# Kernel tuning notes

Measured on AMD Instinct MI355X. Metric: run time of the kernel, lower is better.

Reference implementation:

```python
import jax, jax.numpy as jnp
import numpy as np

LAMBDA_SCR = 0.015
LAMBDA_IFD = 0.015


def setup_inputs() -> dict:
    key = jax.random.key(0)
    k = jax.random.split(key, 5)
    pred = jax.random.normal(k[0], (32, 1000), dtype=jnp.float32)
    feat0 = jax.random.normal(k[1], (32, 64, 128, 128), dtype=jnp.float32)
    feat1 = jax.random.normal(k[2], (32, 128, 64, 64), dtype=jnp.float32)
    feat2 = jax.random.normal(k[3], (32, 256, 32, 32), dtype=jnp.float32)  # teacher
    target = jax.random.randint(k[4], (32,), 0, 1000, dtype=jnp.int64)
    return {"pred": pred, "feat0": feat0, "feat1": feat1, "feat2": feat2, "target": target}


def _adaptive_avg_pool2d(x, out_hw):
    # Exact-multiple adaptive average pool (matches torch for integer ratios).
    B, C, H, W = x.shape
    Ho, Wo = out_hw
    if Ho >= H:
        x = jnp.repeat(x, Ho // H, axis=2)  # replication upsample
    else:
        x = x.reshape(B, C, Ho, H // Ho, W).mean(axis=3)
    if Wo >= W:
        x = jnp.repeat(x, Wo // W, axis=3)
    else:
        x = x.reshape(B, C, x.shape[2], Wo, W // Wo).mean(axis=4)
    return x


def _random_channel_selection(feat, target_channels, key):
    C = feat.shape[1]
    if C == target_channels:
        return feat
    idx = jax.random.permutation(key, C)[:target_channels]
    return feat[:, idx, :, :]


def _ifd_loss(feat):
    B, C, H, W = feat.shape
    if C < 2:
        return jnp.float32(0.0)
    # L2 norm per channel -> descending sort of channel indices
    norms = jnp.linalg.norm(feat.reshape(B, C, H * W), axis=-1)  # [B, C]
    idx = jnp.argsort(-norms, axis=1)                            # [B, C]
    half = C // 2
    strong = jnp.take_along_axis(feat, idx[:, :half, None, None], axis=1)
    weak = jnp.take_along_axis(feat, idx[:, half:2 * half, None, None], axis=1)
    A_strong = jax.nn.sigmoid(strong.mean(axis=1))  # [B, H, W]
    A_weak = jax.nn.sigmoid(weak.mean(axis=1))
    # sum_b mean_hw(diff^2) / B == mean over all elements
    return jnp.mean((A_weak - jax.lax.stop_gradient(A_strong)) ** 2)


def reference(pred, feat0, feat1, feat2, target):
    logp = jax.nn.log_softmax(pred, axis=-1)
    l_main = -jnp.mean(jnp.take_along_axis(logp, target[:, None], axis=1))

    features = [feat0, feat1, feat2]
    teacher = features[-1]
    students = features[:-1]

    sel_key = jax.random.key(42)  # fixed keys stand in for torch.randperm
    l_scr = jnp.float32(0.0)
    for i, student in enumerate(students):
        t_down = _adaptive_avg_pool2d(teacher, student.shape[2:])
        min_C = min(teacher.shape[1], student.shape[1])
        ks, kt = jax.random.split(jax.random.fold_in(sel_key, i))
        s_aligned = _random_channel_selection(student, min_C, ks)
        t_aligned = _random_channel_selection(t_down, min_C, kt)
        l_scr = l_scr + jnp.mean((s_aligned - jax.lax.stop_gradient(t_aligned)) ** 2)
    l_scr = l_scr / len(students)

    l_ifd = jnp.float32(0.0)
    for feat in features:
        l_ifd = l_ifd + _ifd_loss(feat)
    l_ifd = l_ifd / len(features)

    total = l_main + LAMBDA_SCR * l_scr + LAMBDA_IFD * l_ifd
    return (total, l_main, l_scr, l_ifd)
```

## Files before the change

### kernel.cpp

```cpp
#include <hip/hip_runtime.h>
#include <stdint.h>
#include <math.h>

__device__ __forceinline__ void tf_block(uint32_t k0, uint32_t k1, uint32_t& x0, uint32_t& x1) {
  uint32_t k2 = 0x1BD11BDAu ^ k0 ^ k1;
  x0 += k0; x1 += k1;
#define TFR(r) { x0 += x1; x1 = (x1 << r) | (x1 >> (32 - r)); x1 ^= x0; }
  TFR(13) TFR(15) TFR(26) TFR(6)
  x0 += k1; x1 += k2 + 1u;
  TFR(17) TFR(29) TFR(16) TFR(24)
  x0 += k2; x1 += k0 + 2u;
  TFR(13) TFR(15) TFR(26) TFR(6)
  x0 += k0; x1 += k1 + 3u;
  TFR(17) TFR(29) TFR(16) TFR(24)
  x0 += k1; x1 += k2 + 4u;
  TFR(13) TFR(15) TFR(26) TFR(6)
  x0 += k2; x1 += k0 + 5u;
#undef TFR
}

__device__ __forceinline__ float sigmoidf(float x) { return 1.0f / (1.0f + expf(-x)); }

__device__ __forceinline__ float block_reduce(float v, float* red) {
  __syncthreads();
  int lane = threadIdx.x & 63, wv = threadIdx.x >> 6;
  for (int o = 32; o > 0; o >>= 1) v += __shfl_down(v, o, 64);
  if (lane == 0) red[wv] = v;
  __syncthreads();
  float r = 0.f;
  if (threadIdx.x == 0) r = red[0] + red[1] + red[2] + red[3];
  return r;
}

__global__ __launch_bounds__(256) void k0_perm(int* idx0, int* idx1, float* ws, float* totz) {
  int t = threadIdx.x;
  if (blockIdx.x > 0) {
    float4 z = {0.f, 0.f, 0.f, 0.f};
    ((float4*)totz)[(blockIdx.x - 1) * 256 + t] = z;
    return;
  }
  __shared__ uint32_t sub[2][2];
  __shared__ uint32_t bits[2][256];
  for (int i = t; i < 384; i += 256) ws[i] = 0.0f;
  if (t == 0) {
    for (int i = 0; i < 2; ++i) {
      uint32_t f0 = 0u, f1 = (uint32_t)i;
      tf_block(0u, 42u, f0, f1);
      uint32_t a0 = 0u, a1 = 2u; tf_block(f0, f1, a0, a1);
      uint32_t b0 = 1u, b1 = 3u; tf_block(f0, f1, b0, b1);
      uint32_t kt0 = a1, kt1 = b1;
      uint32_t c0 = 0u, c1 = 2u; tf_block(kt0, kt1, c0, c1);
      uint32_t d0 = 1u, d1 = 3u; tf_block(kt0, kt1, d0, d1);
      sub[i][0] = c1; sub[i][1] = d1;
    }
  }
  __syncthreads();
  if (t < 128) {
    for (int i = 0; i < 2; ++i) {
      uint32_t x0 = (uint32_t)t, x1 = (uint32_t)(t + 128);
      tf_block(sub[i][0], sub[i][1], x0, x1);
      bits[i][t] = x0; bits[i][t + 128] = x1;
    }
  }
  __syncthreads();
  for (int i = 0; i < 2; ++i) {
    uint32_t mine = bits[i][t];
    int rank = 0;
    for (int k = 0; k < 256; ++k) {
      uint32_t v = bits[i][k];
      rank += (v < mine) || (v == mine && k < t);
    }
    int lim = (i == 0) ? 64 : 128;
    if (rank < lim) { (i == 0 ? idx0 : idx1)[rank] = t; }
  }
}

template<bool WT>
__global__ __launch_bounds__(256) void k1_pass1(
    const float* __restrict__ f0, const float* __restrict__ f1, const float* __restrict__ f2,
    const int* __restrict__ idx0, const int* __restrict__ idx1,
    float* __restrict__ ns0p, float* __restrict__ ns1p, float* __restrict__ ns2p,
    float* __restrict__ scr0_s, float* __restrict__ scr1_s,
    float* __restrict__ tot0, float* __restrict__ tot1, float* __restrict__ tot2) {
  __shared__ float nsp[16 * 256];
  __shared__ int sidx[128];
  __shared__ float red[8];
  int bid = blockIdx.x, t = threadIdx.x;
  int lane = t & 63, wv = t >> 6;

  if (bid < 2048) {
    int q = bid, b = q >> 6, r = q & 63, chunk = r >> 2, cg = r & 3;
    if (t < 64) sidx[t] = idx0[t];
    __syncthreads();
    const float* fb = f0 + (size_t)b * 1048576 + (size_t)cg * 16 * 16384 + chunk * 1024;
    const float* tb = f2 + (size_t)b * 262144 + (chunk * 2 + (t >> 7)) * 32 + (t & 31);
    float4 tot = {0.f, 0.f, 0.f, 0.f};
    float scr = 0.f;
    #pragma unroll
    for (int c = 0; c < 16; ++c) {
      float4 v = ((const float4*)(fb + (size_t)c * 16384))[t];
      float tv = tb[(size_t)sidx[cg * 16 + c] * 1024];
      tot.x += v.x; tot.y += v.y; tot.z += v.z; tot.w += v.w;
      nsp[c * 256 + t] = v.x * v.x + v.y * v.y + v.z * v.z + v.w * v.w;
      float dx = v.x - tv, dy = v.y - tv, dz = v.z - tv, dw = v.w - tv;
      scr += dx * dx + dy * dy + dz * dz + dw * dw;
    }
    __syncthreads();
    #pragma unroll
    for (int j = 0; j < 4; ++j) {
      int c = wv * 4 + j;
      float s = nsp[c * 256 + lane] + nsp[c * 256 + lane + 64] +
                nsp[c * 256 + lane + 128] + nsp[c * 256 + lane + 192];
      #pragma unroll
      for (int o = 32; o > 0; o >>= 1) s += __shfl_down(s, o, 64);
      if (lane == 0) ns0p[(b * 16 + chunk) * 64 + cg * 16 + c] = s;
    }
    if (WT) {
      float* tp = tot0 + (size_t)b * 16384 + chunk * 1024 + t * 4;
      atomicAdd(tp, tot.x); atomicAdd(tp + 1, tot.y);
      atomicAdd(tp + 2, tot.z); atomicAdd(tp + 3, tot.w);
    }
    float rr = block_reduce(scr, red);
    if (t == 0) atomicAdd(&scr0_s[q & 63], rr);

  } else if (bid < 3072) {
    int q = bid - 2048, b = q >> 5, r = q & 31, chunk = r >> 3, cg = r & 7;
    if (t < 128) sidx[t] = idx1[t];
    __syncthreads();
    const float* fb = f1 + (size_t)b * 524288 + (size_t)cg * 16 * 4096 + chunk * 1024;
    const float* tb = f2 + (size_t)b * 262144 + (chunk * 8 + (t >> 5)) * 32 + (t & 15) * 2;
    float4 tot = {0.f, 0.f, 0.f, 0.f};
    float scr = 0.f;
    #pragma unroll
    for (int c = 0; c < 16; ++c) {
      float4 v = ((const float4*)(fb + (size_t)c * 4096))[t];
      float2 tv = *(const float2*)(tb + (size_t)sidx[cg * 16 + c] * 1024);
      tot.x += v.x; tot.y += v.y; tot.z += v.z; tot.w += v.w;
      nsp[c * 256 + t] = v.x * v.x + v.y * v.y + v.z * v.z + v.w * v.w;
      float dx = v.x - tv.x, dy = v.y - tv.x, dz = v.z - tv.y, dw = v.w - tv.y;
      scr += dx * dx + dy * dy + dz * dz + dw * dw;
    }
    __syncthreads();
    #pragma unroll
    for (int j = 0; j < 4; ++j) {
      int c = wv * 4 + j;
      float s = nsp[c * 256 + lane] + nsp[c * 256 + lane + 64] +
                nsp[c * 256 + lane + 128] + nsp[c * 256 + lane + 192];
      #pragma unroll
      for (int o = 32; o > 0; o >>= 1) s += __shfl_down(s, o, 64);
      if (lane == 0) ns1p[(b * 4 + chunk) * 128 + cg * 16 + c] = s;
    }
    if (WT) {
      float* tp = tot1 + (size_t)b * 4096 + chunk * 1024 + t * 4;
      atomicAdd(tp, tot.x); atomicAdd(tp + 1, tot.y);
      atomicAdd(tp + 2, tot.z); atomicAdd(tp + 3, tot.w);
    }
    float rr = block_reduce(scr, red);
    if (t == 0) atomicAdd(&scr1_s[q & 63], rr);

  } else {
    int q = bid - 3072, b = q >> 4, cg = q & 15;
    const float* fb = f2 + (size_t)b * 262144 + (size_t)cg * 16 * 1024;
    float4 tot = {0.f, 0.f, 0.f, 0.f};
    #pragma unroll
    for (int c = 0; c < 16; ++c) {
      float4 v = ((const float4*)(fb + (size_t)c * 1024))[t];
      tot.x += v.x; tot.y += v.y; tot.z += v.z; tot.w += v.w;
      nsp[c * 256 + t] = v.x * v.x + v.y * v.y + v.z * v.z + v.w * v.w;
    }
    __syncthreads();
    #pragma unroll
    for (int j = 0; j < 4; ++j) {
      int c = wv * 4 + j;
      float s = nsp[c * 256 + lane] + nsp[c * 256 + lane + 64] +
                nsp[c * 256 + lane + 128] + nsp[c * 256 + lane + 192];
      #pragma unroll
      for (int o = 32; o > 0; o >>= 1) s += __shfl_down(s, o, 64);
      if (lane == 0) ns2p[b * 256 + cg * 16 + c] = s;
    }
    if (WT) {
      float* tp = tot2 + (size_t)b * 1024 + t * 4;
      atomicAdd(tp, tot.x); atomicAdd(tp + 1, tot.y);
      atomicAdd(tp + 2, tot.z); atomicAdd(tp + 3, tot.w);
    }
  }
}

template<int C, int NP>
__device__ __forceinline__ void rank_work(const float* __restrict__ nspg,
                                          int* __restrict__ widx, int b, float* nm) {
  int t = threadIdx.x;
  if (t < C) {
    float s = 0.f;
    #pragma unroll
    for (int p = 0; p < NP; ++p) s += nspg[(b * NP + p) * C + t];
    nm[t] = sqrtf(s);
  }
  __syncthreads();
  if (t < C) {
    float mine = nm[t];
    int rank = 0;
    for (int k = 0; k < C; ++k) {
      float v = nm[k];
      rank += (v > mine) || (v == mine && k < t);
    }
    constexpr int HALF = C / 2;
    if (rank >= HALF) widx[b * HALF + rank - HALF] = t;
  }
}

__device__ __forceinline__ void main_work(const float* __restrict__ pred,
                                          const int* __restrict__ target,
                                          float* acc, int b, float* sh) {
  int t = threadIdx.x;
  const float* row = pred + b * 1000;
  float m = -INFINITY;
  for (int j = t; j < 1000; j += 256) m = fmaxf(m, row[j]);
  sh[t] = m; __syncthreads();
  for (int s = 128; s > 0; s >>= 1) { if (t < s) sh[t] = fmaxf(sh[t], sh[t + s]); __syncthreads(); }
  m = sh[0]; __syncthreads();
  float e = 0.f;
  for (int j = t; j < 1000; j += 256) e += expf(row[j] - m);
  sh[t] = e; __syncthreads();
  for (int s = 128; s > 0; s >>= 1) { if (t < s) sh[t] += sh[t + s]; __syncthreads(); }
  if (t == 0) atomicAdd(acc, (logf(sh[0]) + m - row[target[b]]) * (1.0f / 32.0f));
}

__global__ __launch_bounds__(256) void k2_rank_main(
    const float* __restrict__ ns0p, const float* __restrict__ ns1p, const float* __restrict__ ns2p,
    int* __restrict__ widx0, int* __restrict__ widx1, int* __restrict__ widx2,
    const float* __restrict__ pred, const int* __restrict__ target, float* __restrict__ main_acc) {
  __shared__ float sh[256];
  int bid = blockIdx.x;
  if (bid < 32)       rank_work<64, 16>(ns0p, widx0, bid, sh);
  else if (bid < 64)  rank_work<128, 4>(ns1p, widx1, bid - 32, sh);
  else if (bid < 96)  rank_work<256, 1>(ns2p, widx2, bid - 64, sh);
  else                main_work(pred, target, main_acc, bid - 96, sh);
}

template<int C, int HW, bool WT>
__device__ __forceinline__ void ifd_work(const float* __restrict__ feat,
                                         const int* __restrict__ widx,
                                         const float* __restrict__ tot,
                                         float* __restrict__ slots,
                                         int q, int* swx, float* wf, float* red) {
  constexpr int HALF = C / 2;
  constexpr int S2 = HW / 2;
  constexpr int NCH = HW / 512;
  const float ih = 1.0f / (float)HALF;
  int b = q / NCH, ch = q % NCH;
  int t = threadIdx.x;
  const float2* base2 = (const float2*)(feat + (size_t)b * C * HW + ch * 512);
  float2 wk = {0.f, 0.f}, tt = {0.f, 0.f};
  if (WT) {
    if (t < HALF) swx[t] = widx[b * HALF + t];
    __syncthreads();
    #pragma unroll 8
    for (int i = 0; i < HALF; ++i) {
      float2 v = base2[(size_t)swx[i] * S2 + t];
      wk.x += v.x; wk.y += v.y;
    }
    tt = ((const float2*)(tot + (size_t)b * HW + ch * 512))[t];
  } else {
    for (int c = t; c < C; c += 256) wf[c] = 0.f;
    __syncthreads();
    if (t < HALF) wf[widx[b * HALF + t]] = 1.f;
    __syncthreads();
    #pragma unroll 4
    for (int c = 0; c < C; ++c) {
      float2 v = base2[(size_t)c * S2 + t];
      float f = wf[c];
      tt.x += v.x; tt.y += v.y;
      wk.x = fmaf(v.x, f, wk.x); wk.y = fmaf(v.y, f, wk.y);
    }
  }
  float s = 0.f, d;
  d = sigmoidf(wk.x * ih) - sigmoidf((tt.x - wk.x) * ih); s += d * d;
  d = sigmoidf(wk.y * ih) - sigmoidf((tt.y - wk.y) * ih); s += d * d;
  float r = block_reduce(s, red);
  if (t == 0) atomicAdd(&slots[q & 63], r);
}

template<bool WT>
__global__ __launch_bounds__(256) void k3_pass2(
    const float* __restrict__ f0, const float* __restrict__ f1, const float* __restrict__ f2,
    const int* __restrict__ widx0, const int* __restrict__ widx1, const int* __restrict__ widx2,
    const float* __restrict__ tot0, const float* __restrict__ tot1, const float* __restrict__ tot2,
    float* __restrict__ ifd0_s, float* __restrict__ ifd1_s, float* __restrict__ ifd2_s) {
  __shared__ int swx[128];
  __shared__ float wf[256];
  __shared__ float red[8];
  int bid = blockIdx.x;
  if (bid < 64)        ifd_work<256, 1024, WT>(f2, widx2, tot2, ifd2_s, bid, swx, wf, red);
  else if (bid < 320)  ifd_work<128, 4096, WT>(f1, widx1, tot1, ifd1_s, bid - 64, swx, wf, red);
  else                 ifd_work<64, 16384, WT>(f0, widx0, tot0, ifd0_s, bid - 320, swx, wf, red);
}

__global__ void k4_finalize(const float* __restrict__ ws, float* __restrict__ out) {
  float scr0 = 0.f, scr1 = 0.f, ifd0 = 0.f, ifd1 = 0.f, ifd2 = 0.f;
  for (int i = 0; i < 64; ++i) {
    scr0 += ws[i];       scr1 += ws[64 + i];
    ifd0 += ws[128 + i]; ifd1 += ws[192 + i]; ifd2 += ws[256 + i];
  }
  float l_main = ws[320];
  scr0 *= (1.0f / (32.0f * 64.0f * 128.0f * 128.0f));
  scr1 *= (1.0f / (32.0f * 128.0f * 64.0f * 64.0f));
  float l_scr = 0.5f * (scr0 + scr1);
  ifd0 *= (1.0f / (32.0f * 128.0f * 128.0f));
  ifd1 *= (1.0f / (32.0f * 64.0f * 64.0f));
  ifd2 *= (1.0f / (32.0f * 32.0f * 32.0f));
  float l_ifd = (ifd0 + ifd1 + ifd2) * (1.0f / 3.0f);
  float total = l_main + 0.015f * l_scr + 0.015f * l_ifd;
  out[0] = total; out[1] = l_main; out[2] = l_scr; out[3] = l_ifd;
}

extern "C" void kernel_launch(void* const* d_in, const int* in_sizes, int n_in,
                              void* d_out, int out_size, void* d_ws, size_t ws_size,
                              hipStream_t stream) {
  (void)in_sizes; (void)n_in; (void)out_size;
  const float* pred   = (const float*)d_in[0];
  const float* feat0  = (const float*)d_in[1];
  const float* feat1  = (const float*)d_in[2];
  const float* feat2  = (const float*)d_in[3];
  const int*   target = (const int*)d_in[4];
  float* out = (float*)d_out;

  float* ws     = (float*)d_ws;
  float* scr0_s = ws;
  float* scr1_s = ws + 64;
  float* ifd0_s = ws + 128;
  float* ifd1_s = ws + 192;
  float* ifd2_s = ws + 256;
  int*   idx0   = (int*)(ws + 384);
  int*   idx1   = idx0 + 64;
  int*   widx0  = idx1 + 128;
  int*   widx1  = widx0 + 1024;
  int*   widx2  = widx1 + 2048;
  float* ns0p   = (float*)(widx2 + 4096);
  float* ns1p   = ns0p + 32768;
  float* ns2p   = ns1p + 16384;
  float* tot0   = ns2p + 8192;
  float* tot1   = tot0 + 524288;
  float* tot2   = tot1 + 131072;
  const size_t need_full = (size_t)753216 * 4;
  bool wt = (ws_size == 0) || (ws_size >= need_full);

  k0_perm<<<wt ? 673 : 1, 256, 0, stream>>>(idx0, idx1, ws, tot0);
  if (wt) {
    k1_pass1<true><<<3584, 256, 0, stream>>>(feat0, feat1, feat2, idx0, idx1,
                                             ns0p, ns1p, ns2p, scr0_s, scr1_s, tot0, tot1, tot2);
    k2_rank_main<<<128, 256, 0, stream>>>(ns0p, ns1p, ns2p, widx0, widx1, widx2,
                                          pred, target, ws + 320);
    k3_pass2<true><<<1344, 256, 0, stream>>>(feat0, feat1, feat2, widx0, widx1, widx2,
                                             tot0, tot1, tot2, ifd0_s, ifd1_s, ifd2_s);
  } else {
    k1_pass1<false><<<3584, 256, 0, stream>>>(feat0, feat1, feat2, idx0, idx1,
                                              ns0p, ns1p, ns2p, scr0_s, scr1_s, tot0, tot1, tot2);
    k2_rank_main<<<128, 256, 0, stream>>>(ns0p, ns1p, ns2p, widx0, widx1, widx2,
                                          pred, target, ws + 320);
    k3_pass2<false><<<1344, 256, 0, stream>>>(feat0, feat1, feat2, widx0, widx1, widx2,
                                              tot0, tot1, tot2, ifd0_s, ifd1_s, ifd2_s);
  }
  k4_finalize<<<1, 1, 0, stream>>>(ws, out);
}
```

Baseline: 313.5 us.

## Fuse pass1, rank, pass2 and finalize into one persistent kernel with grid barriers

Replaces the four-kernel pipeline with a single persistent kernel of 512 blocks that loops over work items and uses atomic-counter grid barriers between the stat pass, the per-batch channel ranking, the IFD pass and the final reduction. It also adds a tier that writes per-channel-group partial channel sums with plain stores instead of atomics, which the second pass then sums, and it stores per-item partials rather than contended atomic slots. The aim is to remove kernel-launch gaps and atomic contention. In exchange it depends on every block being co-resident for the spin barrier to be safe, uses a bounded spin that could silently break correctness, and reduces parallelism in each phase to 512 blocks.

```diff
diff --git a/kernel.cpp b/kernel.cpp
--- a/kernel.cpp
+++ b/kernel.cpp
@@ -1,6 +1,21 @@
 #include <hip/hip_runtime.h>
 #include <stdint.h>
 #include <math.h>
+
+#define NBLK 512
+
+#define OFF_SCRP   0
+#define OFF_MAINP  3072
+#define OFF_IFDP   3104
+#define OFF_ARR    4512
+#define OFF_IDX    4520
+#define OFF_WIDX0  4712
+#define OFF_WIDX1  5736
+#define OFF_WIDX2  7784
+#define OFF_NS0    11880
+#define OFF_NS1    13928
+#define OFF_NS2    18024
+#define OFF_TOT    26216
 
 __device__ __forceinline__ void tf_block(uint32_t k0, uint32_t k1, uint32_t& x0, uint32_t& x1) {
   uint32_t k2 = 0x1BD11BDAu ^ k0 ^ k1;
@@ -32,16 +47,29 @@
   return r;
 }
 
-__global__ __launch_bounds__(256) void k0_perm(int* idx0, int* idx1, float* ws, float* totz) {
-  int t = threadIdx.x;
-  if (blockIdx.x > 0) {
-    float4 z = {0.f, 0.f, 0.f, 0.f};
-    ((float4*)totz)[(blockIdx.x - 1) * 256 + t] = z;
-    return;
-  }
+__device__ __forceinline__ void gsync(int* arrive, int target) {
+  __syncthreads();
+  if (threadIdx.x == 0) {
+    __hip_atomic_fetch_add(arrive, 1, __ATOMIC_RELEASE, __HIP_MEMORY_SCOPE_AGENT);
+    int spins = 0;
+    while (__hip_atomic_load(arrive, __ATOMIC_RELAXED, __HIP_MEMORY_SCOPE_AGENT) < target) {
+      __builtin_amdgcn_s_sleep(8);
+      if (++spins > 4000000) break;
+    }
+    __threadfence();
+  }
+  __syncthreads();
+}
+
+__global__ __launch_bounds__(256) void k0_perm(float* ws) {
   __shared__ uint32_t sub[2][2];
   __shared__ uint32_t bits[2][256];
-  for (int i = t; i < 384; i += 256) ws[i] = 0.0f;
+  int t = threadIdx.x;
+  float4* nz = (float4*)(ws + OFF_NS0);
+  for (int i = t; i < 3584; i += 256) nz[i] = float4{0.f, 0.f, 0.f, 0.f};
+  if (t == 0) *(int*)(ws + OFF_ARR) = 0;
+  int* idx0 = (int*)(ws + OFF_IDX);
+  int* idx1 = idx0 + 64;
   if (t == 0) {
     for (int i = 0; i < 2; ++i) {
       uint32_t f0 = 0u, f1 = (uint32_t)i;
@@ -75,243 +103,330 @@
   }
 }
 
-template<bool WT>
-__global__ __launch_bounds__(256) void k1_pass1(
+template<int TIER>
+__global__ __launch_bounds__(256, 2) void kfused(
     const float* __restrict__ f0, const float* __restrict__ f1, const float* __restrict__ f2,
-    const int* __restrict__ idx0, const int* __restrict__ idx1,
-    float* __restrict__ ns0p, float* __restrict__ ns1p, float* __restrict__ ns2p,
-    float* __restrict__ scr0_s, float* __restrict__ scr1_s,
-    float* __restrict__ tot0, float* __restrict__ tot1, float* __restrict__ tot2) {
-  __shared__ float nsp[16 * 256];
+    const float* __restrict__ pred, const int* __restrict__ target,
+    float* __restrict__ ws, float* __restrict__ out) {
+  __shared__ float nsp[4096];
   __shared__ int sidx[128];
   __shared__ float red[8];
-  int bid = blockIdx.x, t = threadIdx.x;
-  int lane = t & 63, wv = t >> 6;
-
-  if (bid < 2048) {
-    int q = bid, b = q >> 6, r = q & 63, chunk = r >> 2, cg = r & 3;
-    if (t < 64) sidx[t] = idx0[t];
+  const int bid = blockIdx.x, t = threadIdx.x;
+  const int lane = t & 63, wv = t >> 6;
+
+  float* scrp  = ws + OFF_SCRP;
+  float* mainp = ws + OFF_MAINP;
+  float* ifdp  = ws + OFF_IFDP;
+  int* arrive  = (int*)(ws + OFF_ARR);
+  const int* idxg = (const int*)(ws + OFF_IDX);
+  int* widx0 = (int*)(ws + OFF_WIDX0);
+  int* widx1 = (int*)(ws + OFF_WIDX1);
+  int* widx2 = (int*)(ws + OFF_WIDX2);
+  float* ns0 = ws + OFF_NS0;
+  float* ns1 = ws + OFF_NS1;
+  float* ns2 = ws + OFF_NS2;
+  float* totb = ws + OFF_TOT;
+  int bar = 0;
+
+  if (TIER == 1) {
+    for (int i = bid * 256 + t; i < 172032; i += NBLK * 256)
+      ((float4*)totb)[i] = float4{0.f, 0.f, 0.f, 0.f};
+    gsync(arrive, NBLK * (++bar));
+  }
+
+  for (int item = bid; item < 3616; item += NBLK) {
     __syncthreads();
-    const float* fb = f0 + (size_t)b * 1048576 + (size_t)cg * 16 * 16384 + chunk * 1024;
-    const float* tb = f2 + (size_t)b * 262144 + (chunk * 2 + (t >> 7)) * 32 + (t & 31);
-    float4 tot = {0.f, 0.f, 0.f, 0.f};
-    float scr = 0.f;
-    #pragma unroll
-    for (int c = 0; c < 16; ++c) {
-      float4 v = ((const float4*)(fb + (size_t)c * 16384))[t];
-      float tv = tb[(size_t)sidx[cg * 16 + c] * 1024];
-      tot.x += v.x; tot.y += v.y; tot.z += v.z; tot.w += v.w;
-      nsp[c * 256 + t] = v.x * v.x + v.y * v.y + v.z * v.z + v.w * v.w;
-      float dx = v.x - tv, dy = v.y - tv, dz = v.z - tv, dw = v.w - tv;
-      scr += dx * dx + dy * dy + dz * dz + dw * dw;
-    }
+    if (item < 2048) {
+      int q = item, b = q >> 6, r = q & 63, chunk = r >> 2, cg_ = r & 3;
+      if (t < 16) sidx[t] = idxg[cg_ * 16 + t];
+      __syncthreads();
+      const float* fb = f0 + (size_t)b * 1048576 + (size_t)cg_ * 262144 + chunk * 1024;
+      const float* tb = f2 + (size_t)b * 262144 + (chunk * 2 + (t >> 7)) * 32 + (t & 31);
+      float4 tot = {0.f, 0.f, 0.f, 0.f};
+      float scr = 0.f;
+      #pragma unroll
+      for (int c = 0; c < 16; ++c) {
+        float4 v = ((const float4*)(fb + (size_t)c * 16384))[t];
+        float tv = tb[(size_t)sidx[c] * 1024];
+        tot.x += v.x; tot.y += v.y; tot.z += v.z; tot.w += v.w;
+        nsp[c * 256 + t] = v.x * v.x + v.y * v.y + v.z * v.z + v.w * v.w;
+        float dx = v.x - tv, dy = v.y - tv, dz = v.z - tv, dw = v.w - tv;
+        scr += dx * dx + dy * dy + dz * dz + dw * dw;
+      }
+      __syncthreads();
+      #pragma unroll
+      for (int j = 0; j < 4; ++j) {
+        int c = wv * 4 + j;
+        float s = nsp[c * 256 + lane] + nsp[c * 256 + lane + 64] +
+                  nsp[c * 256 + lane + 128] + nsp[c * 256 + lane + 192];
+        #pragma unroll
+        for (int o = 32; o > 0; o >>= 1) s += __shfl_down(s, o, 64);
+        if (lane == 0) atomicAdd(&ns0[b * 64 + cg_ * 16 + c], s);
+      }
+      if (TIER == 2) {
+        ((float4*)(totb + (size_t)cg_ * 524288 + (size_t)b * 16384 + chunk * 1024))[t] = tot;
+      } else if (TIER == 1) {
+        float* tp = totb + (size_t)b * 16384 + chunk * 1024 + t * 4;
+        atomicAdd(tp, tot.x); atomicAdd(tp + 1, tot.y);
+        atomicAdd(tp + 2, tot.z); atomicAdd(tp + 3, tot.w);
+      }
+      float rr = block_reduce(scr, red);
+      if (t == 0) scrp[item] = rr;
+
+    } else if (item < 3072) {
+      int q = item - 2048, b = q >> 5, r = q & 31, chunk = r >> 3, cg_ = r & 7;
+      if (t < 16) sidx[t] = idxg[64 + cg_ * 16 + t];
+      __syncthreads();
+      const float* fb = f1 + (size_t)b * 524288 + (size_t)cg_ * 65536 + chunk * 1024;
+      const float* tb = f2 + (size_t)b * 262144 + (chunk * 8 + (t >> 5)) * 32 + (t & 15) * 2;
+      float4 tot = {0.f, 0.f, 0.f, 0.f};
+      float scr = 0.f;
+      #pragma unroll
+      for (int c = 0; c < 16; ++c) {
+        float4 v = ((const float4*)(fb + (size_t)c * 4096))[t];
+        float2 tv = *(const float2*)(tb + (size_t)sidx[c] * 1024);
+        tot.x += v.x; tot.y += v.y; tot.z += v.z; tot.w += v.w;
+        nsp[c * 256 + t] = v.x * v.x + v.y * v.y + v.z * v.z + v.w * v.w;
+        float dx = v.x - tv.x, dy = v.y - tv.x, dz = v.z - tv.y, dw = v.w - tv.y;
+        scr += dx * dx + dy * dy + dz * dz + dw * dw;
+      }
+      __syncthreads();
+      #pragma unroll
+      for (int j = 0; j < 4; ++j) {
+        int c = wv * 4 + j;
+        float s = nsp[c * 256 + lane] + nsp[c * 256 + lane + 64] +
+                  nsp[c * 256 + lane + 128] + nsp[c * 256 + lane + 192];
+        #pragma unroll
+        for (int o = 32; o > 0; o >>= 1) s += __shfl_down(s, o, 64);
+        if (lane == 0) atomicAdd(&ns1[b * 128 + cg_ * 16 + c], s);
+      }
+      if (TIER == 2) {
+        ((float4*)(totb + 2097152 + (size_t)cg_ * 131072 + (size_t)b * 4096 + chunk * 1024))[t] = tot;
+      } else if (TIER == 1) {
+        float* tp = totb + 524288 + (size_t)b * 4096 + chunk * 1024 + t * 4;
+        atomicAdd(tp, tot.x); atomicAdd(tp + 1, tot.y);
+        atomicAdd(tp + 2, tot.z); atomicAdd(tp + 3, tot.w);
+      }
+      float rr = block_reduce(scr, red);
+      if (t == 0) scrp[item] = rr;
+
+    } else if (item < 3584) {
+      int q = item - 3072, b = q >> 4, cg_ = q & 15;
+      const float* fb = f2 + (size_t)b * 262144 + (size_t)cg_ * 16384;
+      float4 tot = {0.f, 0.f, 0.f, 0.f};
+      #pragma unroll
+      for (int c = 0; c < 16; ++c) {
+        float4 v = ((const float4*)(fb + (size_t)c * 1024))[t];
+        tot.x += v.x; tot.y += v.y; tot.z += v.z; tot.w += v.w;
+        nsp[c * 256 + t] = v.x * v.x + v.y * v.y + v.z * v.z + v.w * v.w;
+      }
+      __syncthreads();
+      #pragma unroll
+      for (int j = 0; j < 4; ++j) {
+        int c = wv * 4 + j;
+        float s = nsp[c * 256 + lane] + nsp[c * 256 + lane + 64] +
+                  nsp[c * 256 + lane + 128] + nsp[c * 256 + lane + 192];
+        #pragma unroll
+        for (int o = 32; o > 0; o >>= 1) s += __shfl_down(s, o, 64);
+        if (lane == 0) ns2[b * 256 + cg_ * 16 + c] = s;
+      }
+      if (TIER == 2) {
+        ((float4*)(totb + 3145728 + (size_t)cg_ * 32768 + (size_t)b * 1024))[t] = tot;
+      } else if (TIER == 1) {
+        float* tp = totb + 655360 + (size_t)b * 1024 + t * 4;
+        atomicAdd(tp, tot.x); atomicAdd(tp + 1, tot.y);
+        atomicAdd(tp + 2, tot.z); atomicAdd(tp + 3, tot.w);
+      }
+
+    } else {
+      int b = item - 3584;
+      const float* row = pred + b * 1000;
+      float m = -INFINITY;
+      for (int j = t; j < 1000; j += 256) m = fmaxf(m, row[j]);
+      nsp[t] = m; __syncthreads();
+      for (int s = 128; s > 0; s >>= 1) { if (t < s) nsp[t] = fmaxf(nsp[t], nsp[t + s]); __syncthreads(); }
+      m = nsp[0]; __syncthreads();
+      float e = 0.f;
+      for (int j = t; j < 1000; j += 256) e += expf(row[j] - m);
+      nsp[t] = e; __syncthreads();
+      for (int s = 128; s > 0; s >>= 1) { if (t < s) nsp[t] += nsp[t + s]; __syncthreads(); }
+      if (t == 0) mainp[b] = logf(nsp[0]) + m - row[target[b]];
+    }
+  }
+  gsync(arrive, NBLK * (++bar));
+
+  if (bid < 96) {
+    float* nm = nsp;
+    float* wk = nsp + 256;
+    const float* nsg; int* widx; int C, b;
+    if (bid < 32)      { nsg = ns0; widx = widx0; C = 64;  b = bid; }
+    else if (bid < 64) { nsg = ns1; widx = widx1; C = 128; b = bid - 32; }
+    else               { nsg = ns2; widx = widx2; C = 256; b = bid - 64; }
+    if (t < C) nm[t] = sqrtf(nsg[b * C + t]);
     __syncthreads();
-    #pragma unroll
-    for (int j = 0; j < 4; ++j) {
-      int c = wv * 4 + j;
-      float s = nsp[c * 256 + lane] + nsp[c * 256 + lane + 64] +
-                nsp[c * 256 + lane + 128] + nsp[c * 256 + lane + 192];
-      #pragma unroll
-      for (int o = 32; o > 0; o >>= 1) s += __shfl_down(s, o, 64);
-      if (lane == 0) ns0p[(b * 16 + chunk) * 64 + cg * 16 + c] = s;
-    }
-    if (WT) {
-      float* tp = tot0 + (size_t)b * 16384 + chunk * 1024 + t * 4;
-      atomicAdd(tp, tot.x); atomicAdd(tp + 1, tot.y);
-      atomicAdd(tp + 2, tot.z); atomicAdd(tp + 3, tot.w);
-    }
-    float rr = block_reduce(scr, red);
-    if (t == 0) atomicAdd(&scr0_s[q & 63], rr);
-
-  } else if (bid < 3072) {
-    int q = bid - 2048, b = q >> 5, r = q & 31, chunk = r >> 3, cg = r & 7;
-    if (t < 128) sidx[t] = idx1[t];
+    if (t < C) {
+      float mine = nm[t];
+      int rank = 0;
+      for (int k = 0; k < C; ++k) {
+        float v = nm[k];
+        rank += (v > mine) || (v == mine && k < t);
+      }
+      wk[t] = (rank >= C / 2) ? 1.f : 0.f;
+    }
     __syncthreads();
-    const float* fb = f1 + (size_t)b * 524288 + (size_t)cg * 16 * 4096 + chunk * 1024;
-    const float* tb = f2 + (size_t)b * 262144 + (chunk * 8 + (t >> 5)) * 32 + (t & 15) * 2;
-    float4 tot = {0.f, 0.f, 0.f, 0.f};
-    float scr = 0.f;
-    #pragma unroll
-    for (int c = 0; c < 16; ++c) {
-      float4 v = ((const float4*)(fb + (size_t)c * 4096))[t];
-      float2 tv = *(const float2*)(tb + (size_t)sidx[cg * 16 + c] * 1024);
-      tot.x += v.x; tot.y += v.y; tot.z += v.z; tot.w += v.w;
-      nsp[c * 256 + t] = v.x * v.x + v.y * v.y + v.z * v.z + v.w * v.w;
-      float dx = v.x - tv.x, dy = v.y - tv.x, dz = v.z - tv.y, dw = v.w - tv.y;
-      scr += dx * dx + dy * dy + dz * dz + dw * dw;
-    }
+    if (t < C && wk[t] > 0.5f) {
+      int pos = 0;
+      for (int k = 0; k < t; ++k) pos += (int)wk[k];
+      widx[b * (C / 2) + pos] = t;
+    }
+  }
+  gsync(arrive, NBLK * (++bar));
+
+  for (int i = bid; i < 1408; i += NBLK) {
     __syncthreads();
-    #pragma unroll
-    for (int j = 0; j < 4; ++j) {
-      int c = wv * 4 + j;
-      float s = nsp[c * 256 + lane] + nsp[c * 256 + lane + 64] +
-                nsp[c * 256 + lane + 128] + nsp[c * 256 + lane + 192];
-      #pragma unroll
-      for (int o = 32; o > 0; o >>= 1) s += __shfl_down(s, o, 64);
-      if (lane == 0) ns1p[(b * 4 + chunk) * 128 + cg * 16 + c] = s;
-    }
-    if (WT) {
-      float* tp = tot1 + (size_t)b * 4096 + chunk * 1024 + t * 4;
-      atomicAdd(tp, tot.x); atomicAdd(tp + 1, tot.y);
-      atomicAdd(tp + 2, tot.z); atomicAdd(tp + 3, tot.w);
-    }
-    float rr = block_reduce(scr, red);
-    if (t == 0) atomicAdd(&scr1_s[q & 63], rr);
-
-  } else {
-    int q = bid - 3072, b = q >> 4, cg = q & 15;
-    const float* fb = f2 + (size_t)b * 262144 + (size_t)cg * 16 * 1024;
-    float4 tot = {0.f, 0.f, 0.f, 0.f};
-    #pragma unroll
-    for (int c = 0; c < 16; ++c) {
-      float4 v = ((const float4*)(fb + (size_t)c * 1024))[t];
-      tot.x += v.x; tot.y += v.y; tot.z += v.z; tot.w += v.w;
-      nsp[c * 256 + t] = v.x * v.x + v.y * v.y + v.z * v.z + v.w * v.w;
-    }
-    __syncthreads();
-    #pragma unroll
-    for (int j = 0; j < 4; ++j) {
-      int c = wv * 4 + j;
-      float s = nsp[c * 256 + lane] + nsp[c * 256 + lane + 64] +
-                nsp[c * 256 + lane + 128] + nsp[c * 256 + lane + 192];
-      #pragma unroll
-      for (int o = 32; o > 0; o >>= 1) s += __shfl_down(s, o, 64);
-      if (lane == 0) ns2p[b * 256 + cg * 16 + c] = s;
-    }
-    if (WT) {
-      float* tp = tot2 + (size_t)b * 1024 + t * 4;
-      atomicAdd(tp, tot.x); atomicAdd(tp + 1, tot.y);
-      atomicAdd(tp + 2, tot.z); atomicAdd(tp + 3, tot.w);
-    }
-  }
-}
-
-template<int C, int NP>
-__device__ __forceinline__ void rank_work(const float* __restrict__ nspg,
-                                          int* __restrict__ widx, int b, float* nm) {
-  int t = threadIdx.x;
-  if (t < C) {
-    float s = 0.f;
-    #pragma unroll
-    for (int p = 0; p < NP; ++p) s += nspg[(b * NP + p) * C + t];
-    nm[t] = sqrtf(s);
-  }
-  __syncthreads();
-  if (t < C) {
-    float mine = nm[t];
-    int rank = 0;
-    for (int k = 0; k < C; ++k) {
-      float v = nm[k];
-      rank += (v > mine) || (v == mine && k < t);
-    }
-    constexpr int HALF = C / 2;
-    if (rank >= HALF) widx[b * HALF + rank - HALF] = t;
-  }
-}
-
-__device__ __forceinline__ void main_work(const float* __restrict__ pred,
-                                          const int* __restrict__ target,
-                                          float* acc, int b, float* sh) {
-  int t = threadIdx.x;
-  const float* row = pred + b * 1000;
-  float m = -INFINITY;
-  for (int j = t; j < 1000; j += 256) m = fmaxf(m, row[j]);
-  sh[t] = m; __syncthreads();
-  for (int s = 128; s > 0; s >>= 1) { if (t < s) sh[t] = fmaxf(sh[t], sh[t + s]); __syncthreads(); }
-  m = sh[0]; __syncthreads();
-  float e = 0.f;
-  for (int j = t; j < 1000; j += 256) e += expf(row[j] - m);
-  sh[t] = e; __syncthreads();
-  for (int s = 128; s > 0; s >>= 1) { if (t < s) sh[t] += sh[t + s]; __syncthreads(); }
-  if (t == 0) atomicAdd(acc, (logf(sh[0]) + m - row[target[b]]) * (1.0f / 32.0f));
-}
-
-__global__ __launch_bounds__(256) void k2_rank_main(
-    const float* __restrict__ ns0p, const float* __restrict__ ns1p, const float* __restrict__ ns2p,
-    int* __restrict__ widx0, int* __restrict__ widx1, int* __restrict__ widx2,
-    const float* __restrict__ pred, const int* __restrict__ target, float* __restrict__ main_acc) {
-  __shared__ float sh[256];
-  int bid = blockIdx.x;
-  if (bid < 32)       rank_work<64, 16>(ns0p, widx0, bid, sh);
-  else if (bid < 64)  rank_work<128, 4>(ns1p, widx1, bid - 32, sh);
-  else if (bid < 96)  rank_work<256, 1>(ns2p, widx2, bid - 64, sh);
-  else                main_work(pred, target, main_acc, bid - 96, sh);
-}
-
-template<int C, int HW, bool WT>
-__device__ __forceinline__ void ifd_work(const float* __restrict__ feat,
-                                         const int* __restrict__ widx,
-                                         const float* __restrict__ tot,
-                                         float* __restrict__ slots,
-                                         int q, int* swx, float* wf, float* red) {
-  constexpr int HALF = C / 2;
-  constexpr int S2 = HW / 2;
-  constexpr int NCH = HW / 512;
-  const float ih = 1.0f / (float)HALF;
-  int b = q / NCH, ch = q % NCH;
-  int t = threadIdx.x;
-  const float2* base2 = (const float2*)(feat + (size_t)b * C * HW + ch * 512);
-  float2 wk = {0.f, 0.f}, tt = {0.f, 0.f};
-  if (WT) {
-    if (t < HALF) swx[t] = widx[b * HALF + t];
-    __syncthreads();
-    #pragma unroll 8
-    for (int i = 0; i < HALF; ++i) {
-      float2 v = base2[(size_t)swx[i] * S2 + t];
-      wk.x += v.x; wk.y += v.y;
-    }
-    tt = ((const float2*)(tot + (size_t)b * HW + ch * 512))[t];
-  } else {
-    for (int c = t; c < C; c += 256) wf[c] = 0.f;
-    __syncthreads();
-    if (t < HALF) wf[widx[b * HALF + t]] = 1.f;
-    __syncthreads();
-    #pragma unroll 4
-    for (int c = 0; c < C; ++c) {
-      float2 v = base2[(size_t)c * S2 + t];
-      float f = wf[c];
-      tt.x += v.x; tt.y += v.y;
-      wk.x = fmaf(v.x, f, wk.x); wk.y = fmaf(v.y, f, wk.y);
-    }
-  }
-  float s = 0.f, d;
-  d = sigmoidf(wk.x * ih) - sigmoidf((tt.x - wk.x) * ih); s += d * d;
-  d = sigmoidf(wk.y * ih) - sigmoidf((tt.y - wk.y) * ih); s += d * d;
-  float r = block_reduce(s, red);
-  if (t == 0) atomicAdd(&slots[q & 63], r);
-}
-
-template<bool WT>
-__global__ __launch_bounds__(256) void k3_pass2(
-    const float* __restrict__ f0, const float* __restrict__ f1, const float* __restrict__ f2,
-    const int* __restrict__ widx0, const int* __restrict__ widx1, const int* __restrict__ widx2,
-    const float* __restrict__ tot0, const float* __restrict__ tot1, const float* __restrict__ tot2,
-    float* __restrict__ ifd0_s, float* __restrict__ ifd1_s, float* __restrict__ ifd2_s) {
-  __shared__ int swx[128];
-  __shared__ float wf[256];
-  __shared__ float red[8];
-  int bid = blockIdx.x;
-  if (bid < 64)        ifd_work<256, 1024, WT>(f2, widx2, tot2, ifd2_s, bid, swx, wf, red);
-  else if (bid < 320)  ifd_work<128, 4096, WT>(f1, widx1, tot1, ifd1_s, bid - 64, swx, wf, red);
-  else                 ifd_work<64, 16384, WT>(f0, widx0, tot0, ifd0_s, bid - 320, swx, wf, red);
-}
-
-__global__ void k4_finalize(const float* __restrict__ ws, float* __restrict__ out) {
-  float scr0 = 0.f, scr1 = 0.f, ifd0 = 0.f, ifd1 = 0.f, ifd2 = 0.f;
-  for (int i = 0; i < 64; ++i) {
-    scr0 += ws[i];       scr1 += ws[64 + i];
-    ifd0 += ws[128 + i]; ifd1 += ws[192 + i]; ifd2 += ws[256 + i];
-  }
-  float l_main = ws[320];
-  scr0 *= (1.0f / (32.0f * 64.0f * 128.0f * 128.0f));
-  scr1 *= (1.0f / (32.0f * 128.0f * 64.0f * 64.0f));
-  float l_scr = 0.5f * (scr0 + scr1);
-  ifd0 *= (1.0f / (32.0f * 128.0f * 128.0f));
-  ifd1 *= (1.0f / (32.0f * 64.0f * 64.0f));
-  ifd2 *= (1.0f / (32.0f * 32.0f * 32.0f));
-  float l_ifd = (ifd0 + ifd1 + ifd2) * (1.0f / 3.0f);
-  float total = l_main + 0.015f * l_scr + 0.015f * l_ifd;
-  out[0] = total; out[1] = l_main; out[2] = l_scr; out[3] = l_ifd;
+    if (i < 128) {
+      int b = i >> 2, qtr = i & 3;
+      if (t < 128) sidx[t] = widx2[b * 128 + t];
+      __syncthreads();
+      const float* base = f2 + (size_t)b * 262144 + qtr * 256;
+      float wkv = 0.f, tt = 0.f;
+      if (TIER > 0) {
+        #pragma unroll 8
+        for (int k = 0; k < 128; ++k) wkv += base[(size_t)sidx[k] * 1024 + t];
+        if (TIER == 2) {
+          #pragma unroll
+          for (int p = 0; p < 16; ++p) tt += totb[3145728 + (size_t)p * 32768 + b * 1024 + qtr * 256 + t];
+        } else {
+          tt = totb[655360 + (size_t)b * 1024 + qtr * 256 + t];
+        }
+      } else {
+        float* wf = nsp;
+        wf[t] = 0.f;
+        __syncthreads();
+        if (t < 128) wf[sidx[t]] = 1.f;
+        __syncthreads();
+        #pragma unroll 4
+        for (int c = 0; c < 256; ++c) {
+          float v = base[(size_t)c * 1024 + t];
+          tt += v; wkv = fmaf(v, wf[c], wkv);
+        }
+      }
+      float d = sigmoidf(wkv * (1.f / 128.f)) - sigmoidf((tt - wkv) * (1.f / 128.f));
+      float r = block_reduce(d * d, red);
+      if (t == 0) ifdp[i] = r;
+
+    } else if (i < 384) {
+      int q = i - 128, b = q >> 3, ch = q & 7;
+      if (t < 64) sidx[t] = widx1[b * 64 + t];
+      __syncthreads();
+      const float2* base2 = (const float2*)(f1 + (size_t)b * 524288 + ch * 512);
+      float2 wk2 = {0.f, 0.f}, tt2 = {0.f, 0.f};
+      if (TIER > 0) {
+        #pragma unroll 8
+        for (int k = 0; k < 64; ++k) {
+          float2 v = base2[(size_t)sidx[k] * 2048 + t];
+          wk2.x += v.x; wk2.y += v.y;
+        }
+        if (TIER == 2) {
+          #pragma unroll
+          for (int p = 0; p < 8; ++p) {
+            float2 v = ((const float2*)(totb + 2097152 + (size_t)p * 131072 + (size_t)b * 4096 + ch * 512))[t];
+            tt2.x += v.x; tt2.y += v.y;
+          }
+        } else {
+          tt2 = ((const float2*)(totb + 524288 + (size_t)b * 4096 + ch * 512))[t];
+        }
+      } else {
+        float* wf = nsp;
+        if (t < 128) wf[t] = 0.f;
+        __syncthreads();
+        if (t < 64) wf[sidx[t]] = 1.f;
+        __syncthreads();
+        #pragma unroll 4
+        for (int c = 0; c < 128; ++c) {
+          float2 v = base2[(size_t)c * 2048 + t];
+          float f = wf[c];
+          tt2.x += v.x; tt2.y += v.y;
+          wk2.x = fmaf(v.x, f, wk2.x); wk2.y = fmaf(v.y, f, wk2.y);
+        }
+      }
+      float s = 0.f, d;
+      d = sigmoidf(wk2.x * (1.f / 64.f)) - sigmoidf((tt2.x - wk2.x) * (1.f / 64.f)); s += d * d;
+      d = sigmoidf(wk2.y * (1.f / 64.f)) - sigmoidf((tt2.y - wk2.y) * (1.f / 64.f)); s += d * d;
+      float r = block_reduce(s, red);
+      if (t == 0) ifdp[i] = r;
+
+    } else {
+      int q = i - 384, b = q >> 5, ch = q & 31;
+      if (t < 32) sidx[t] = widx0[b * 32 + t];
+      __syncthreads();
+      const float2* base2 = (const float2*)(f0 + (size_t)b * 1048576 + ch * 512);
+      float2 wk2 = {0.f, 0.f}, tt2 = {0.f, 0.f};
+      if (TIER > 0) {
+        #pragma unroll 8
+        for (int k = 0; k < 32; ++k) {
+          float2 v = base2[(size_t)sidx[k] * 8192 + t];
+          wk2.x += v.x; wk2.y += v.y;
+        }
+        if (TIER == 2) {
+          #pragma unroll
+          for (int p = 0; p < 4; ++p) {
+            float2 v = ((const float2*)(totb + (size_t)p * 524288 + (size_t)b * 16384 + ch * 512))[t];
+            tt2.x += v.x; tt2.y += v.y;
+          }
+        } else {
+          tt2 = ((const float2*)(totb + (size_t)b * 16384 + ch * 512))[t];
+        }
+      } else {
+        float* wf = nsp;
+        if (t < 64) wf[t] = 0.f;
+        __syncthreads();
+        if (t < 32) wf[sidx[t]] = 1.f;
+        __syncthreads();
+        #pragma unroll 4
+        for (int c = 0; c < 64; ++c) {
+          float2 v = base2[(size_t)c * 8192 + t];
+          float f = wf[c];
+          tt2.x += v.x; tt2.y += v.y;
+          wk2.x = fmaf(v.x, f, wk2.x); wk2.y = fmaf(v.y, f, wk2.y);
+        }
+      }
+      float s = 0.f, d;
+      d = sigmoidf(wk2.x * (1.f / 32.f)) - sigmoidf((tt2.x - wk2.x) * (1.f / 32.f)); s += d * d;
+      d = sigmoidf(wk2.y * (1.f / 32.f)) - sigmoidf((tt2.y - wk2.y) * (1.f / 32.f)); s += d * d;
+      float r = block_reduce(s, red);
+      if (t == 0) ifdp[i] = r;
+    }
+  }
+  gsync(arrive, NBLK * (++bar));
+
+  if (bid == 0) {
+    float s0 = 0.f, s1 = 0.f, i0 = 0.f, i1 = 0.f, i2 = 0.f, mn = 0.f;
+    for (int i = t; i < 2048; i += 256) s0 += scrp[i];
+    for (int i = 2048 + t; i < 3072; i += 256) s1 += scrp[i];
+    for (int i = t; i < 128; i += 256) i2 += ifdp[i];
+    for (int i = 128 + t; i < 384; i += 256) i1 += ifdp[i];
+    for (int i = 384 + t; i < 1408; i += 256) i0 += ifdp[i];
+    if (t < 32) mn = mainp[t];
+    s0 = block_reduce(s0, red);
+    s1 = block_reduce(s1, red);
+    i0 = block_reduce(i0, red);
+    i1 = block_reduce(i1, red);
+    i2 = block_reduce(i2, red);
+    mn = block_reduce(mn, red);
+    if (t == 0) {
+      float scr0 = s0 * (1.0f / (32.0f * 64.0f * 128.0f * 128.0f));
+      float scr1 = s1 * (1.0f / (32.0f * 128.0f * 64.0f * 64.0f));
+      float l_scr = 0.5f * (scr0 + scr1);
+      float ifd0 = i0 * (1.0f / (32.0f * 128.0f * 128.0f));
+      float ifd1 = i1 * (1.0f / (32.0f * 64.0f * 64.0f));
+      float ifd2 = i2 * (1.0f / (32.0f * 32.0f * 32.0f));
+      float l_ifd = (ifd0 + ifd1 + ifd2) * (1.0f / 3.0f);
+      float l_main = mn * (1.0f / 32.0f);
+      out[0] = l_main + 0.015f * l_scr + 0.015f * l_ifd;
+      out[1] = l_main; out[2] = l_scr; out[3] = l_ifd;
+    }
+  }
 }
 
 extern "C" void kernel_launch(void* const* d_in, const int* in_sizes, int n_in,
@@ -323,43 +438,18 @@
   const float* feat1  = (const float*)d_in[2];
   const float* feat2  = (const float*)d_in[3];
   const int*   target = (const int*)d_in[4];
+  float* ws  = (float*)d_ws;
   float* out = (float*)d_out;
 
-  float* ws     = (float*)d_ws;
-  float* scr0_s = ws;
-  float* scr1_s = ws + 64;
-  float* ifd0_s = ws + 128;
-  float* ifd1_s = ws + 192;
-  float* ifd2_s = ws + 256;
-  int*   idx0   = (int*)(ws + 384);
-  int*   idx1   = idx0 + 64;
-  int*   widx0  = idx1 + 128;
-  int*   widx1  = widx0 + 1024;
-  int*   widx2  = widx1 + 2048;
-  float* ns0p   = (float*)(widx2 + 4096);
-  float* ns1p   = ns0p + 32768;
-  float* ns2p   = ns1p + 16384;
-  float* tot0   = ns2p + 8192;
-  float* tot1   = tot0 + 524288;
-  float* tot2   = tot1 + 131072;
-  const size_t need_full = (size_t)753216 * 4;
-  bool wt = (ws_size == 0) || (ws_size >= need_full);
-
-  k0_perm<<<wt ? 673 : 1, 256, 0, stream>>>(idx0, idx1, ws, tot0);
-  if (wt) {
-    k1_pass1<true><<<3584, 256, 0, stream>>>(feat0, feat1, feat2, idx0, idx1,
-                                             ns0p, ns1p, ns2p, scr0_s, scr1_s, tot0, tot1, tot2);
-    k2_rank_main<<<128, 256, 0, stream>>>(ns0p, ns1p, ns2p, widx0, widx1, widx2,
-                                          pred, target, ws + 320);
-    k3_pass2<true><<<1344, 256, 0, stream>>>(feat0, feat1, feat2, widx0, widx1, widx2,
-                                             tot0, tot1, tot2, ifd0_s, ifd1_s, ifd2_s);
+  const size_t need_T1 = (size_t)(OFF_TOT + 688128) * 4;
+  const size_t need_T2 = (size_t)(OFF_TOT + 3670016) * 4;
+
+  k0_perm<<<1, 256, 0, stream>>>(ws);
+  if (ws_size >= need_T2) {
+    kfused<2><<<NBLK, 256, 0, stream>>>(feat0, feat1, feat2, pred, target, ws, out);
+  } else if (ws_size == 0 || ws_size >= need_T1) {
+    kfused<1><<<NBLK, 256, 0, stream>>>(feat0, feat1, feat2, pred, target, ws, out);
   } else {
-    k1_pass1<false><<<3584, 256, 0, stream>>>(feat0, feat1, feat2, idx0, idx1,
-                                              ns0p, ns1p, ns2p, scr0_s, scr1_s, tot0, tot1, tot2);
-    k2_rank_main<<<128, 256, 0, stream>>>(ns0p, ns1p, ns2p, widx0, widx1, widx2,
-                                          pred, target, ws + 320);
-    k3_pass2<false><<<1344, 256, 0, stream>>>(feat0, feat1, feat2, widx0, widx1, widx2,
-                                              tot0, tot1, tot2, ifd0_s, ifd1_s, ifd2_s);
-  }
-  k4_finalize<<<1, 1, 0, stream>>>(ws, out);
-}
+    kfused<0><<<NBLK, 256, 0, stream>>>(feat0, feat1, feat2, pred, target, ws, out);
+  }
+}
```

New measurement: 435.1 us. +38.8%, slower.
